# Performance work log

Measured on AMD Instinct MI355X. Metric: run time of the kernel, lower is better.

## Reference

```python
import jax, jax.numpy as jnp
import numpy as np

N = 100000
E = 1600000
D_IN = 128
D_H = 128


def setup_inputs() -> dict:
    key = jax.random.key(0)
    ks = jax.random.split(key, 8)
    x = jax.random.normal(ks[0], (N, D_IN), dtype=jnp.float32)
    edge_index = jax.random.randint(ks[1], (2, E), 0, N, dtype=jnp.int64)
    # Glorot-ish init for weights, zeros for biases (PyG GCNConv default: glorot W, zero bias)
    W1 = jax.random.normal(ks[2], (D_IN, D_H), dtype=jnp.float32) / np.sqrt(D_IN)
    b1 = jnp.zeros((D_H,), dtype=jnp.float32)
    W2 = jax.random.normal(ks[3], (D_H, D_H), dtype=jnp.float32) / np.sqrt(D_H)
    b2 = jnp.zeros((D_H,), dtype=jnp.float32)
    Wout = jax.random.normal(ks[4], (D_H, 1), dtype=jnp.float32) / np.sqrt(D_H)
    bout = jnp.zeros((1,), dtype=jnp.float32)
    return {"x": x, "edge_index": edge_index, "W1": W1, "b1": b1,
            "W2": W2, "b2": b2, "Wout": Wout, "bout": bout}


def _gcn_conv(x, W, b, src, dst, inv_sqrt_deg, inv_deg):
    # PyG GCNConv: h = x @ W; out = sum_{j in N(i)} norm_ij * h_j + (1/deg_i) * h_i + b
    # norm_ij = deg_i^-1/2 * deg_j^-1/2 with self-loops folded into deg.
    h = x @ W                                   # [N, D]
    norm = inv_sqrt_deg[src] * inv_sqrt_deg[dst]  # [E]
    msgs = h[src] * norm[:, None]               # [E, D] gather
    agg = jax.ops.segment_sum(msgs, dst, num_segments=x.shape[0])  # [N, D] scatter
    agg = agg + h * inv_deg[:, None]            # self-loop term (norm = 1/deg)
    return agg + b


def reference(x, edge_index, W1, b1, W2, b2, Wout, bout):
    src = edge_index[0]
    dst = edge_index[1]
    n = x.shape[0]
    # degree with self-loops: deg_i = 1 + #incoming edges to i
    deg = 1.0 + jax.ops.segment_sum(jnp.ones((src.shape[0],), dtype=x.dtype), dst, num_segments=n)
    inv_sqrt_deg = jax.lax.rsqrt(deg)
    inv_deg = 1.0 / deg
    h = jax.nn.relu(_gcn_conv(x, W1, b1, src, dst, inv_sqrt_deg, inv_deg))
    h = jax.nn.relu(_gcn_conv(h, W2, b2, src, dst, inv_sqrt_deg, inv_deg))
    logits = h @ Wout + bout                    # [N, 1]
    return jax.nn.sigmoid(logits).squeeze(-1)   # [N]
```

## Files before the change

kernel.cpp:

```cpp
#include <hip/hip_runtime.h>
#include <cstddef>

#define CAPD 64
#define BSZ 512
#define BSH 9
#define CHUNK 8192
#define BCAP 12288

typedef unsigned int uint;
typedef unsigned short ushort;
typedef unsigned char uchar;
typedef float f32x4 __attribute__((ext_vector_type(4)));
typedef _Float16 f16x8 __attribute__((ext_vector_type(8)));

__device__ inline float h_lo(uint v) {
    union { ushort u; _Float16 h; } c; c.u = (ushort)(v & 0xFFFFu); return (float)c.h;
}
__device__ inline float h_hi(uint v) {
    union { ushort u; _Float16 h; } c; c.u = (ushort)(v >> 16); return (float)c.h;
}
__device__ inline ushort h_bits(float x) {
    union { _Float16 h; ushort u; } c; c.h = (_Float16)x; return c.u;
}
__device__ inline uint h_pack(float a, float b) {
    return (uint)h_bits(a) | ((uint)h_bits(b) << 16);
}
__device__ inline float ub0(uint v) { return (float)(v & 0xFFu); }
__device__ inline float ub1(uint v) { return (float)((v >> 8) & 0xFFu); }
__device__ inline float ub2(uint v) { return (float)((v >> 16) & 0xFFu); }
__device__ inline float ub3(uint v) { return (float)(v >> 24); }

__global__ __launch_bounds__(256) void p3_scatter(const int* __restrict__ esrc,
                                                  const int* __restrict__ edst, int E,
                                                  int nb, int NB2,
                                                  int* __restrict__ bucketCursor,
                                                  unsigned* __restrict__ gSorted,
                                                  const float* __restrict__ W1,
                                                  const float* __restrict__ W2,
                                                  uint* __restrict__ Wt1,
                                                  uint* __restrict__ Wt2) {
    __shared__ __align__(16) char SHB[78848];
    int bid = blockIdx.x, tid = threadIdx.x;
    if (bid >= NB2) {
        const float* W = (bid - NB2) ? W2 : W1;
        uint* O = (bid - NB2) ? Wt2 : Wt1;
        float (*ws)[129] = (float(*)[129])SHB;
#pragma unroll
        for (int j = 0; j < 16; ++j) {
            int q = tid + 256 * j;
            int k = q >> 5, c = (q & 31) * 4;
            float4 v = *reinterpret_cast<const float4*>(W + k * 128 + c);
            ws[k][c] = v.x; ws[k][c + 1] = v.y; ws[k][c + 2] = v.z; ws[k][c + 3] = v.w;
        }
        __syncthreads();
#pragma unroll
        for (int j = 0; j < 32; ++j) {
            int q = tid + 256 * j;
            int ncol = q >> 6, kw = q & 63;
            O[q] = h_pack(ws[2 * kw][ncol], ws[2 * kw + 1][ncol]);
        }
        return;
    }
    uint*  payL = (uint*)SHB;
    uint*  outL = (uint*)(SHB + 32768);
    uchar* bktL = (uchar*)(SHB + 65536);
    int*   hist   = (int*)(SHB + 73728);
    int*   segoff = hist + 256;
    int*   cursor = segoff + 256;
    int*   gbase  = cursor + 256;
    int*   sc     = gbase + 256;
    int e0 = bid * CHUNK;
    int m = min(E - e0, CHUNK);
    for (int i = tid; i < m; i += 256) {
        unsigned d = (unsigned)edst[e0 + i];
        unsigned s = (unsigned)esrc[e0 + i];
        payL[i] = s | ((d & (BSZ - 1)) << 23);
        bktL[i] = (uchar)(d >> BSH);
    }
    hist[tid] = 0;
    __syncthreads();
    for (int i = tid; i < m; i += 256)
        atomicAdd(&hist[bktL[i]], 1);
    __syncthreads();
    sc[tid] = hist[tid];
    __syncthreads();
    for (int off = 1; off < 256; off <<= 1) {
        int v = (tid >= off) ? sc[tid - off] : 0;
        __syncthreads();
        sc[tid] += v;
        __syncthreads();
    }
    segoff[tid] = sc[tid] - hist[tid];
    cursor[tid] = segoff[tid];
    if (tid < nb && hist[tid] > 0) gbase[tid] = atomicAdd(&bucketCursor[tid], hist[tid]);
    __syncthreads();
    for (int i = tid; i < m; i += 256) {
        int b = (int)bktL[i];
        int p = atomicAdd(&cursor[b], 1);
        outL[p] = payL[i];
    }
    __syncthreads();
    int wave = tid >> 6, lane = tid & 63;
    for (int b = wave; b < nb; b += 4) {
        int off = segoff[b], len = hist[b];
        if (len == 0) continue;
        int gb = gbase[b];
        unsigned* dst = gSorted + (size_t)b * BCAP;
        for (int i = lane; i < len; i += 64)
            if (gb + i < BCAP) dst[gb + i] = outL[off + i];
    }
}

__device__ __forceinline__ void gemm_core(const void* __restrict__ A, int aF16,
                                          const uint* __restrict__ Wt,
                                          const float* __restrict__ scale,
                                          uint* __restrict__ Tq,
                                          float* __restrict__ Ts,
                                          int n, int m0, int tid, uint* SH) {
    char* shb = (char*)SH;
    if (aF16) {
        const uint* Af = (const uint*)A;
#pragma unroll
        for (int j = 0; j < 8; ++j) {
            int q = tid + 256 * j;
            int row = q >> 4, c16 = q & 15;
            int grow = m0 + row;
            uint4 v = make_uint4(0u, 0u, 0u, 0u);
            if (grow < n) v = *reinterpret_cast<const uint4*>(Af + (size_t)grow * 64 + c16 * 4);
            *reinterpret_cast<uint4*>(shb + row * 256 + ((c16 * 16) ^ ((row & 7) << 4))) = v;
        }
    } else {
        const float* Af = (const float*)A;
#pragma unroll
        for (int j = 0; j < 8; ++j) {
            int q = tid + 256 * j;
            int row = q >> 4, c16 = q & 15;
            int grow = m0 + row;
            uint4 o = make_uint4(0u, 0u, 0u, 0u);
            if (grow < n) {
                float4 v0 = *reinterpret_cast<const float4*>(Af + (size_t)grow * 128 + c16 * 8);
                float4 v1 = *reinterpret_cast<const float4*>(Af + (size_t)grow * 128 + c16 * 8 + 4);
                o.x = h_pack(v0.x, v0.y); o.y = h_pack(v0.z, v0.w);
                o.z = h_pack(v1.x, v1.y); o.w = h_pack(v1.z, v1.w);
            }
            *reinterpret_cast<uint4*>(shb + row * 256 + ((c16 * 16) ^ ((row & 7) << 4))) = o;
        }
    }
#pragma unroll
    for (int j = 0; j < 8; ++j) {
        int q = tid + 256 * j;
        int col = q >> 4, c16 = q & 15;
        uint4 v = *reinterpret_cast<const uint4*>(Wt + col * 64 + c16 * 4);
        *reinterpret_cast<uint4*>(shb + 32768 + col * 256 + ((c16 * 16) ^ ((col & 7) << 4))) = v;
    }
    __syncthreads();

    const int w = tid >> 6, l = tid & 63;
    const int lrow = l & 15, kg = l >> 4;
    const int swz = (lrow & 7) << 4;

    f32x4 acc[2][8] = {};
#pragma unroll
    for (int kk = 0; kk < 4; ++kk) {
        const int koff = (kk * 64 + kg * 16) ^ swz;
        f16x8 a[2], b[8];
#pragma unroll
        for (int mr = 0; mr < 2; ++mr) {
            int r = w * 32 + mr * 16 + lrow;
            a[mr] = *reinterpret_cast<const f16x8*>(shb + r * 256 + koff);
        }
#pragma unroll
        for (int nc = 0; nc < 8; ++nc) {
            int c = nc * 16 + lrow;
            b[nc] = *reinterpret_cast<const f16x8*>(shb + 32768 + c * 256 + koff);
        }
#pragma unroll
        for (int mr = 0; mr < 2; ++mr)
#pragma unroll
            for (int nc = 0; nc < 8; ++nc)
                acc[mr][nc] = __builtin_amdgcn_mfma_f32_16x16x32_f16(a[mr], b[nc], acc[mr][nc], 0, 0, 0);
    }
    __syncthreads();

    ushort* Cs = (ushort*)SH;
#pragma unroll
    for (int mr = 0; mr < 2; ++mr) {
        int rb = w * 32 + mr * 16 + kg * 4;
#pragma unroll
        for (int i = 0; i < 4; ++i) {
            int grow = m0 + rb + i;
            float s = scale ? ((grow < n) ? scale[grow] : 0.f) : 1.f;
#pragma unroll
            for (int nc = 0; nc < 8; ++nc)
                Cs[(rb + i) * 136 + nc * 16 + lrow] = h_bits(s * acc[mr][nc][i]);
        }
    }
    __syncthreads();
    const uint* Cw = (const uint*)SH;
#pragma unroll
    for (int j = 0; j < 8; ++j) {
        int q = tid + 256 * j;
        int row = q >> 4, c8 = q & 15;
        int grow = m0 + row;
        uint4 v = *reinterpret_cast<const uint4*>(Cw + row * 68 + c8 * 4);
        float f0 = h_lo(v.x), f1 = h_hi(v.x), f2 = h_lo(v.y), f3 = h_hi(v.y);
        float f4 = h_lo(v.z), f5 = h_hi(v.z), f6 = h_lo(v.w), f7 = h_hi(v.w);
        float mx = fmaxf(fmaxf(fmaxf(fabsf(f0), fabsf(f1)), fmaxf(fabsf(f2), fabsf(f3))),
                         fmaxf(fmaxf(fabsf(f4), fabsf(f5)), fmaxf(fabsf(f6), fabsf(f7))));
#pragma unroll
        for (int off = 8; off > 0; off >>= 1) mx = fmaxf(mx, __shfl_xor(mx, off, 16));
        mx = fmaxf(mx, 1e-20f);
        float inv = 127.f / mx;
        int q0 = (int)rintf(f0 * inv) + 128, q1 = (int)rintf(f1 * inv) + 128;
        int q2 = (int)rintf(f2 * inv) + 128, q3 = (int)rintf(f3 * inv) + 128;
        int q4 = (int)rintf(f4 * inv) + 128, q5 = (int)rintf(f5 * inv) + 128;
        int q6 = (int)rintf(f6 * inv) + 128, q7 = (int)rintf(f7 * inv) + 128;
        uint w0 = (uint)q0 | ((uint)q1 << 8) | ((uint)q2 << 16) | ((uint)q3 << 24);
        uint w1 = (uint)q4 | ((uint)q5 << 8) | ((uint)q6 << 16) | ((uint)q7 << 24);
        if (grow < n) {
            *reinterpret_cast<uint2*>(Tq + (size_t)grow * 32 + c8 * 2) = make_uint2(w0, w1);
            if (c8 == 0) Ts[grow] = mx * (1.f / 127.f);
        }
    }
}

__global__ __launch_bounds__(256) void p4_mega(const unsigned* __restrict__ gSorted,
                                               const int* __restrict__ bucketCursor,
                                               int nb, int N,
                                               int* __restrict__ cnt,
                                               float* __restrict__ isd,
                                               int* __restrict__ ell,
                                               const float* __restrict__ x,
                                               const uint* __restrict__ Wt1,
                                               uint* __restrict__ Tq,
                                               float* __restrict__ Ts) {
    __shared__ __align__(16) uint SH[16384];
    __shared__ int cntL[256];
    int bid = blockIdx.x, tid = threadIdx.x;
    if (bid < 2 * nb) {
        int bucket = bid >> 1;
        unsigned half = (unsigned)(bid & 1);
        int n0 = bid * 256;
        uint* ellL = SH;
        cntL[tid] = 0;
        __syncthreads();
        int len = bucketCursor[bucket];
        if (len > BCAP) len = BCAP;
        const unsigned* seg = gSorted + (size_t)bucket * BCAP;
        for (int i = tid; i < len; i += 256) {
            unsigned e = seg[i];
            unsigned dl = e >> 23;
            if ((dl >> 8) == half) {
                int r = (int)(dl & 255u);
                int p = atomicAdd(&cntL[r], 1);
                if (p < CAPD) ellL[r * CAPD + p] = e & 0x7FFFFFu;
            }
        }
        __syncthreads();
        int nValid = min(256, N - n0);
        if (nValid > 0) {
            int total = nValid * CAPD;
            const int* ellLi = (const int*)ellL;
            for (int i = tid; i < total; i += 256) {
                int row = i >> 6, pos = i & 63;
                int c = cntL[row];
                if (pos < min(c, CAPD))
                    ell[(size_t)n0 * CAPD + i] = ellLi[i];
            }
            for (int i = tid; i < nValid; i += 256) {
                int c = cntL[i];
                cnt[n0 + i] = c;
                isd[n0 + i] = rsqrtf(1.0f + (float)c);
            }
        }
    } else {
        gemm_core(x, 0, Wt1, nullptr, Tq, Ts, N, (bid - 2 * nb) * 128, tid, SH);
    }
}

__global__ __launch_bounds__(256) void tsc_kernel(const float* __restrict__ Ts,
                                                  const float* __restrict__ isd,
                                                  float* __restrict__ Tsc, int n4) {
    int i = (blockIdx.x * 256 + threadIdx.x) * 4;
    if (i >= n4 * 4) return;
    float4 a = *reinterpret_cast<const float4*>(Ts + i);
    float4 b = *reinterpret_cast<const float4*>(isd + i);
    float4 o = make_float4(a.x * b.x, a.y * b.y, a.z * b.z, a.w * b.w);
    *reinterpret_cast<float4*>(Tsc + i) = o;
}

__global__ __launch_bounds__(256) void gemm2_kernel(const uint* __restrict__ Hb,
                                                    const uint* __restrict__ Wt,
                                                    const float* __restrict__ isd,
                                                    uint* __restrict__ Tq,
                                                    float* __restrict__ Ts, int n) {
    __shared__ __align__(16) uint SH[16384];
    gemm_core(Hb, 1, Wt, isd, Tq, Ts, n, blockIdx.x * 128, threadIdx.x, SH);
}

__global__ __launch_bounds__(256) void agg_kernel(const uint* __restrict__ Tq,
                                                  const float* __restrict__ Tsc,
                                                  const int* __restrict__ ell,
                                                  const int* __restrict__ cnt,
                                                  const float* __restrict__ isd,
                                                  const float* __restrict__ bias,
                                                  uint* __restrict__ Hb, int n) {
    int node = (int)((blockIdx.x * 256 + threadIdx.x) >> 5);
    int ln = threadIdx.x & 31;
    if (node >= n) return;
    float di = isd[node];
    int c = cnt[node];
    if (c > CAPD) c = CAPD;
    const int* row = ell + (size_t)node * CAPD;
    float a0, a1, a2, a3, ssum;
    {
        uint v = Tq[(size_t)node * 32 + ln];
        float sc = Tsc[node];
        ssum = sc;
        a0 = sc * ub0(v); a1 = sc * ub1(v); a2 = sc * ub2(v); a3 = sc * ub3(v);
    }
    int j = 0;
    for (; j + 8 <= c; j += 8) {
        int4 sa = *reinterpret_cast<const int4*>(row + j);
        int4 sb = *reinterpret_cast<const int4*>(row + j + 4);
        uint v0 = Tq[(size_t)sa.x * 32 + ln]; float c0 = Tsc[sa.x];
        uint v1 = Tq[(size_t)sa.y * 32 + ln]; float c1 = Tsc[sa.y];
        uint v2 = Tq[(size_t)sa.z * 32 + ln]; float c2 = Tsc[sa.z];
        uint v3 = Tq[(size_t)sa.w * 32 + ln]; float c3 = Tsc[sa.w];
        uint v4 = Tq[(size_t)sb.x * 32 + ln]; float c4 = Tsc[sb.x];
        uint v5 = Tq[(size_t)sb.y * 32 + ln]; float c5 = Tsc[sb.y];
        uint v6 = Tq[(size_t)sb.z * 32 + ln]; float c6 = Tsc[sb.z];
        uint v7 = Tq[(size_t)sb.w * 32 + ln]; float c7 = Tsc[sb.w];
        ssum += ((c0 + c1) + (c2 + c3)) + ((c4 + c5) + (c6 + c7));
        a0 = fmaf(c0, ub0(v0), fmaf(c1, ub0(v1), fmaf(c2, ub0(v2), fmaf(c3, ub0(v3),
             fmaf(c4, ub0(v4), fmaf(c5, ub0(v5), fmaf(c6, ub0(v6), fmaf(c7, ub0(v7), a0))))))));
        a1 = fmaf(c0, ub1(v0), fmaf(c1, ub1(v1), fmaf(c2, ub1(v2), fmaf(c3, ub1(v3),
             fmaf(c4, ub1(v4), fmaf(c5, ub1(v5), fmaf(c6, ub1(v6), fmaf(c7, ub1(v7), a1))))))));
        a2 = fmaf(c0, ub2(v0), fmaf(c1, ub2(v1), fmaf(c2, ub2(v2), fmaf(c3, ub2(v3),
             fmaf(c4, ub2(v4), fmaf(c5, ub2(v5), fmaf(c6, ub2(v6), fmaf(c7, ub2(v7), a2))))))));
        a3 = fmaf(c0, ub3(v0), fmaf(c1, ub3(v1), fmaf(c2, ub3(v2), fmaf(c3, ub3(v3),
             fmaf(c4, ub3(v4), fmaf(c5, ub3(v5), fmaf(c6, ub3(v6), fmaf(c7, ub3(v7), a3))))))));
    }
    for (; j + 4 <= c; j += 4) {
        int4 s4 = *reinterpret_cast<const int4*>(row + j);
        uint v0 = Tq[(size_t)s4.x * 32 + ln]; float c0 = Tsc[s4.x];
        uint v1 = Tq[(size_t)s4.y * 32 + ln]; float c1 = Tsc[s4.y];
        uint v2 = Tq[(size_t)s4.z * 32 + ln]; float c2 = Tsc[s4.z];
        uint v3 = Tq[(size_t)s4.w * 32 + ln]; float c3 = Tsc[s4.w];
        ssum += (c0 + c1) + (c2 + c3);
        a0 = fmaf(c0, ub0(v0), fmaf(c1, ub0(v1), fmaf(c2, ub0(v2), fmaf(c3, ub0(v3), a0))));
        a1 = fmaf(c0, ub1(v0), fmaf(c1, ub1(v1), fmaf(c2, ub1(v2), fmaf(c3, ub1(v3), a1))));
        a2 = fmaf(c0, ub2(v0), fmaf(c1, ub2(v1), fmaf(c2, ub2(v2), fmaf(c3, ub2(v3), a2))));
        a3 = fmaf(c0, ub3(v0), fmaf(c1, ub3(v1), fmaf(c2, ub3(v2), fmaf(c3, ub3(v3), a3))));
    }
    for (; j < c; ++j) {
        int s = row[j];
        uint v = Tq[(size_t)s * 32 + ln];
        float sc = Tsc[s];
        ssum += sc;
        a0 = fmaf(sc, ub0(v), a0); a1 = fmaf(sc, ub1(v), a1);
        a2 = fmaf(sc, ub2(v), a2); a3 = fmaf(sc, ub3(v), a3);
    }
    float off = 128.f * ssum;
    float4 bv = *reinterpret_cast<const float4*>(bias + ln * 4);
    float h0 = fmaxf(fmaf(di, a0 - off, bv.x), 0.f);
    float h1 = fmaxf(fmaf(di, a1 - off, bv.y), 0.f);
    float h2 = fmaxf(fmaf(di, a2 - off, bv.z), 0.f);
    float h3 = fmaxf(fmaf(di, a3 - off, bv.w), 0.f);
    *reinterpret_cast<uint2*>(Hb + (size_t)node * 64 + ln * 2) =
        make_uint2(h_pack(h0, h1), h_pack(h2, h3));
}

__global__ __launch_bounds__(256) void agg_out_kernel(const uint* __restrict__ Tq,
                                                      const float* __restrict__ Ts,
                                                      const int* __restrict__ ell,
                                                      const int* __restrict__ cnt,
                                                      const float* __restrict__ isd,
                                                      const float* __restrict__ bias,
                                                      const float* __restrict__ Wout,
                                                      const float* __restrict__ bout,
                                                      float* __restrict__ out, int n) {
    int node = (int)((blockIdx.x * 256 + threadIdx.x) >> 5);
    int ln = threadIdx.x & 31;
    if (node >= n) return;
    float di = isd[node];
    int c = cnt[node];
    if (c > CAPD) c = CAPD;
    const int* row = ell + (size_t)node * CAPD;
    float a0, a1, a2, a3, ssum;
    {
        uint v = Tq[(size_t)node * 32 + ln];
        float sc = Ts[node];
        ssum = sc;
        a0 = sc * ub0(v); a1 = sc * ub1(v); a2 = sc * ub2(v); a3 = sc * ub3(v);
    }
    int j = 0;
    for (; j + 8 <= c; j += 8) {
        int4 sa = *reinterpret_cast<const int4*>(row + j);
        int4 sb = *reinterpret_cast<const int4*>(row + j + 4);
        uint v0 = Tq[(size_t)sa.x * 32 + ln]; float c0 = Ts[sa.x];
        uint v1 = Tq[(size_t)sa.y * 32 + ln]; float c1 = Ts[sa.y];
        uint v2 = Tq[(size_t)sa.z * 32 + ln]; float c2 = Ts[sa.z];
        uint v3 = Tq[(size_t)sa.w * 32 + ln]; float c3 = Ts[sa.w];
        uint v4 = Tq[(size_t)sb.x * 32 + ln]; float c4 = Ts[sb.x];
        uint v5 = Tq[(size_t)sb.y * 32 + ln]; float c5 = Ts[sb.y];
        uint v6 = Tq[(size_t)sb.z * 32 + ln]; float c6 = Ts[sb.z];
        uint v7 = Tq[(size_t)sb.w * 32 + ln]; float c7 = Ts[sb.w];
        ssum += ((c0 + c1) + (c2 + c3)) + ((c4 + c5) + (c6 + c7));
        a0 = fmaf(c0, ub0(v0), fmaf(c1, ub0(v1), fmaf(c2, ub0(v2), fmaf(c3, ub0(v3),
             fmaf(c4, ub0(v4), fmaf(c5, ub0(v5), fmaf(c6, ub0(v6), fmaf(c7, ub0(v7), a0))))))));
        a1 = fmaf(c0, ub1(v0), fmaf(c1, ub1(v1), fmaf(c2, ub1(v2), fmaf(c3, ub1(v3),
             fmaf(c4, ub1(v4), fmaf(c5, ub1(v5), fmaf(c6, ub1(v6), fmaf(c7, ub1(v7), a1))))))));
        a2 = fmaf(c0, ub2(v0), fmaf(c1, ub2(v1), fmaf(c2, ub2(v2), fmaf(c3, ub2(v3),
             fmaf(c4, ub2(v4), fmaf(c5, ub2(v5), fmaf(c6, ub2(v6), fmaf(c7, ub2(v7), a2))))))));
        a3 = fmaf(c0, ub3(v0), fmaf(c1, ub3(v1), fmaf(c2, ub3(v2), fmaf(c3, ub3(v3),
             fmaf(c4, ub3(v4), fmaf(c5, ub3(v5), fmaf(c6, ub3(v6), fmaf(c7, ub3(v7), a3))))))));
    }
    for (; j + 4 <= c; j += 4) {
        int4 s4 = *reinterpret_cast<const int4*>(row + j);
        uint v0 = Tq[(size_t)s4.x * 32 + ln]; float c0 = Ts[s4.x];
        uint v1 = Tq[(size_t)s4.y * 32 + ln]; float c1 = Ts[s4.y];
        uint v2 = Tq[(size_t)s4.z * 32 + ln]; float c2 = Ts[s4.z];
        uint v3 = Tq[(size_t)s4.w * 32 + ln]; float c3 = Ts[s4.w];
        ssum += (c0 + c1) + (c2 + c3);
        a0 = fmaf(c0, ub0(v0), fmaf(c1, ub0(v1), fmaf(c2, ub0(v2), fmaf(c3, ub0(v3), a0))));
        a1 = fmaf(c0, ub1(v0), fmaf(c1, ub1(v1), fmaf(c2, ub1(v2), fmaf(c3, ub1(v3), a1))));
        a2 = fmaf(c0, ub2(v0), fmaf(c1, ub2(v1), fmaf(c2, ub2(v2), fmaf(c3, ub2(v3), a2))));
        a3 = fmaf(c0, ub3(v0), fmaf(c1, ub3(v1), fmaf(c2, ub3(v2), fmaf(c3, ub3(v3), a3))));
    }
    for (; j < c; ++j) {
        int s = row[j];
        uint v = Tq[(size_t)s * 32 + ln];
        float sc = Ts[s];
        ssum += sc;
        a0 = fmaf(sc, ub0(v), a0); a1 = fmaf(sc, ub1(v), a1);
        a2 = fmaf(sc, ub2(v), a2); a3 = fmaf(sc, ub3(v), a3);
    }
    float off = 128.f * ssum;
    float4 bv = *reinterpret_cast<const float4*>(bias + ln * 4);
    float4 wv = *reinterpret_cast<const float4*>(Wout + ln * 4);
    float h0 = fmaxf(fmaf(di, a0 - off, bv.x), 0.f);
    float h1 = fmaxf(fmaf(di, a1 - off, bv.y), 0.f);
    float h2 = fmaxf(fmaf(di, a2 - off, bv.z), 0.f);
    float h3 = fmaxf(fmaf(di, a3 - off, bv.w), 0.f);
    float v = fmaf(h0, wv.x, fmaf(h1, wv.y, fmaf(h2, wv.z, h3 * wv.w)));
#pragma unroll
    for (int off2 = 16; off2 > 0; off2 >>= 1) v += __shfl_xor(v, off2, 32);
    if (ln == 0) out[node] = 1.f / (1.f + expf(-(v + bout[0])));
}

extern "C" void kernel_launch(void* const* d_in, const int* in_sizes, int n_in,
                              void* d_out, int out_size, void* d_ws, size_t ws_size,
                              hipStream_t stream) {
    const float* x    = (const float*)d_in[0];
    const int*   ei   = (const int*)d_in[1];
    const float* W1   = (const float*)d_in[2];
    const float* b1   = (const float*)d_in[3];
    const float* W2   = (const float*)d_in[4];
    const float* b2   = (const float*)d_in[5];
    const float* Wout = (const float*)d_in[6];
    const float* bout = (const float*)d_in[7];
    float* out = (float*)d_out;

    const int N = in_sizes[0] / 128;
    const int E = in_sizes[1] / 2;
    const int* esrc = ei;
    const int* edst = ei + E;

    char* p = (char*)d_ws;
    auto alloc = [&](size_t bytes) {
        char* r = p;
        p += (bytes + 255) & ~(size_t)255;
        return (void*)r;
    };
    const int nb  = (N + BSZ - 1) / BSZ;
    const int NB2 = (E + CHUNK - 1) / CHUNK;

    int*   cnt = (int*)  alloc((size_t)N * 4);
    float* isd = (float*)alloc((size_t)N * 4);
    int*   ell = (int*)  alloc((size_t)N * CAPD * 4);
    uint*  Tq  = (uint*) alloc((size_t)N * 32 * 4);
    float* Ts  = (float*)alloc((size_t)(N + 4) * 4);
    float* Tsc = (float*)alloc((size_t)(N + 4) * 4);
    uint*  Hb  = (uint*) alloc((size_t)N * 64 * 4);
    uint*  Wt1 = (uint*) alloc(8192 * 4);
    uint*  Wt2 = (uint*) alloc(8192 * 4);
    unsigned* gSorted      = (unsigned*)alloc((size_t)nb * BCAP * 4);
    int*      bucketCursor = (int*)     alloc((size_t)nb * 4);

    hipMemsetAsync(bucketCursor, 0, (size_t)nb * 4, stream);
    p3_scatter<<<NB2 + 2, 256, 0, stream>>>(esrc, edst, E, nb, NB2, bucketCursor, gSorted,
                                            W1, W2, Wt1, Wt2);

    const int gblocks = (N + 127) / 128;
    const int ablocks = (N + 7) / 8;
    p4_mega<<<2 * nb + gblocks, 256, 0, stream>>>(gSorted, bucketCursor, nb, N,
                                                  cnt, isd, ell, x, Wt1, Tq, Ts);
    const int n4 = (N + 3) / 4;
    tsc_kernel<<<(n4 + 255) / 256, 256, 0, stream>>>(Ts, isd, Tsc, n4);
    agg_kernel<<<ablocks, 256, 0, stream>>>(Tq, Tsc, ell, cnt, isd, b1, Hb, N);
    gemm2_kernel<<<gblocks, 256, 0, stream>>>(Hb, Wt2, isd, Tq, Ts, N);
    agg_out_kernel<<<ablocks, 256, 0, stream>>>(Tq, Ts, ell, cnt, isd, b2, Wout, bout, out, N);
}
```

Before: 178.2 us.

## Split ELL build from GEMM1, fuse Tsc scaling into GEMM1 epilogue

The combined ELL-build plus GEMM1 kernel is split in two. A separate ELL build kernel now uses 128-node sub-buckets, four per bucket, so it needs less shared memory and launches more blocks. GEMM1 then runs after it and computes Tsc = Ts*isd directly in its epilogue, which removes the separate tsc kernel launch and its pass over memory. The cost is that the two phases no longer overlap within a single launch, and each bucket segment is now scanned four times instead of twice.

Measured after the change: 188.5 us. +5.7%, slower.

```diff
diff --git a/kernel.cpp b/kernel.cpp
--- a/kernel.cpp
+++ b/kernel.cpp
@@ -111,11 +111,56 @@
     }
 }
 
+__global__ __launch_bounds__(256) void p4_build(const unsigned* __restrict__ gSorted,
+                                                const int* __restrict__ bucketCursor,
+                                                int nb, int N, int* __restrict__ cnt,
+                                                float* __restrict__ isd,
+                                                int* __restrict__ ell) {
+    __shared__ unsigned ellL[128 * CAPD];
+    __shared__ int cntL[128];
+    int bid = blockIdx.x, tid = threadIdx.x;
+    int bucket = bid >> 2;
+    unsigned sub = (unsigned)(bid & 3);
+    int n0 = bid * 128;
+    int nValid = min(128, N - n0);
+    if (nValid <= 0) return;
+    for (int i = tid; i < 128; i += 256) cntL[i] = 0;
+    __syncthreads();
+    int len = bucketCursor[bucket];
+    if (len > BCAP) len = BCAP;
+    const unsigned* seg = gSorted + (size_t)bucket * BCAP;
+    for (int i = tid; i < len; i += 256) {
+        unsigned e = seg[i];
+        unsigned dl = e >> 23;
+        if ((dl >> 7) == sub) {
+            int r = (int)(dl & 127u);
+            int p = atomicAdd(&cntL[r], 1);
+            if (p < CAPD) ellL[r * CAPD + p] = e & 0x7FFFFFu;
+        }
+    }
+    __syncthreads();
+    int total = nValid * CAPD;
+    const int* ellLi = (const int*)ellL;
+    for (int i = tid; i < total; i += 256) {
+        int row = i >> 6, pos = i & 63;
+        int c = cntL[row];
+        if (pos < min(c, CAPD))
+            ell[(size_t)n0 * CAPD + i] = ellLi[i];
+    }
+    for (int i = tid; i < nValid; i += 256) {
+        int c = cntL[i];
+        cnt[n0 + i] = c;
+        isd[n0 + i] = rsqrtf(1.0f + (float)c);
+    }
+}
+
 __device__ __forceinline__ void gemm_core(const void* __restrict__ A, int aF16,
                                           const uint* __restrict__ Wt,
                                           const float* __restrict__ scale,
+                                          const float* __restrict__ isdT,
                                           uint* __restrict__ Tq,
                                           float* __restrict__ Ts,
+                                          float* __restrict__ TscOut,
                                           int n, int m0, int tid, uint* SH) {
     char* shb = (char*)SH;
     if (aF16) {
@@ -219,74 +264,23 @@
         uint w1 = (uint)q4 | ((uint)q5 << 8) | ((uint)q6 << 16) | ((uint)q7 << 24);
         if (grow < n) {
             *reinterpret_cast<uint2*>(Tq + (size_t)grow * 32 + c8 * 2) = make_uint2(w0, w1);
-            if (c8 == 0) Ts[grow] = mx * (1.f / 127.f);
-        }
-    }
-}
-
-__global__ __launch_bounds__(256) void p4_mega(const unsigned* __restrict__ gSorted,
-                                               const int* __restrict__ bucketCursor,
-                                               int nb, int N,
-                                               int* __restrict__ cnt,
-                                               float* __restrict__ isd,
-                                               int* __restrict__ ell,
-                                               const float* __restrict__ x,
-                                               const uint* __restrict__ Wt1,
-                                               uint* __restrict__ Tq,
-                                               float* __restrict__ Ts) {
+            if (c8 == 0) {
+                float ts = mx * (1.f / 127.f);
+                Ts[grow] = ts;
+                if (TscOut) TscOut[grow] = ts * isdT[grow];
+            }
+        }
+    }
+}
+
+__global__ __launch_bounds__(256) void gemm1_kernel(const float* __restrict__ x,
+                                                    const uint* __restrict__ Wt,
+                                                    const float* __restrict__ isd,
+                                                    uint* __restrict__ Tq,
+                                                    float* __restrict__ Ts,
+                                                    float* __restrict__ Tsc, int n) {
     __shared__ __align__(16) uint SH[16384];
-    __shared__ int cntL[256];
-    int bid = blockIdx.x, tid = threadIdx.x;
-    if (bid < 2 * nb) {
-        int bucket = bid >> 1;
-        unsigned half = (unsigned)(bid & 1);
-        int n0 = bid * 256;
-        uint* ellL = SH;
-        cntL[tid] = 0;
-        __syncthreads();
-        int len = bucketCursor[bucket];
-        if (len > BCAP) len = BCAP;
-        const unsigned* seg = gSorted + (size_t)bucket * BCAP;
-        for (int i = tid; i < len; i += 256) {
-            unsigned e = seg[i];
-            unsigned dl = e >> 23;
-            if ((dl >> 8) == half) {
-                int r = (int)(dl & 255u);
-                int p = atomicAdd(&cntL[r], 1);
-                if (p < CAPD) ellL[r * CAPD + p] = e & 0x7FFFFFu;
-            }
-        }
-        __syncthreads();
-        int nValid = min(256, N - n0);
-        if (nValid > 0) {
-            int total = nValid * CAPD;
-            const int* ellLi = (const int*)ellL;
-            for (int i = tid; i < total; i += 256) {
-                int row = i >> 6, pos = i & 63;
-                int c = cntL[row];
-                if (pos < min(c, CAPD))
-                    ell[(size_t)n0 * CAPD + i] = ellLi[i];
-            }
-            for (int i = tid; i < nValid; i += 256) {
-                int c = cntL[i];
-                cnt[n0 + i] = c;
-                isd[n0 + i] = rsqrtf(1.0f + (float)c);
-            }
-        }
-    } else {
-        gemm_core(x, 0, Wt1, nullptr, Tq, Ts, N, (bid - 2 * nb) * 128, tid, SH);
-    }
-}
-
-__global__ __launch_bounds__(256) void tsc_kernel(const float* __restrict__ Ts,
-                                                  const float* __restrict__ isd,
-                                                  float* __restrict__ Tsc, int n4) {
-    int i = (blockIdx.x * 256 + threadIdx.x) * 4;
-    if (i >= n4 * 4) return;
-    float4 a = *reinterpret_cast<const float4*>(Ts + i);
-    float4 b = *reinterpret_cast<const float4*>(isd + i);
-    float4 o = make_float4(a.x * b.x, a.y * b.y, a.z * b.z, a.w * b.w);
-    *reinterpret_cast<float4*>(Tsc + i) = o;
+    gemm_core(x, 0, Wt, nullptr, isd, Tq, Ts, Tsc, n, blockIdx.x * 128, threadIdx.x, SH);
 }
 
 __global__ __launch_bounds__(256) void gemm2_kernel(const uint* __restrict__ Hb,
@@ -295,7 +289,7 @@
                                                     uint* __restrict__ Tq,
                                                     float* __restrict__ Ts, int n) {
     __shared__ __align__(16) uint SH[16384];
-    gemm_core(Hb, 1, Wt, isd, Tq, Ts, n, blockIdx.x * 128, threadIdx.x, SH);
+    gemm_core(Hb, 1, Wt, isd, nullptr, Tq, Ts, nullptr, n, blockIdx.x * 128, threadIdx.x, SH);
 }
 
 __global__ __launch_bounds__(256) void agg_kernel(const uint* __restrict__ Tq,
@@ -491,13 +485,11 @@
     hipMemsetAsync(bucketCursor, 0, (size_t)nb * 4, stream);
     p3_scatter<<<NB2 + 2, 256, 0, stream>>>(esrc, edst, E, nb, NB2, bucketCursor, gSorted,
                                             W1, W2, Wt1, Wt2);
+    p4_build<<<4 * nb, 256, 0, stream>>>(gSorted, bucketCursor, nb, N, cnt, isd, ell);
 
     const int gblocks = (N + 127) / 128;
     const int ablocks = (N + 7) / 8;
-    p4_mega<<<2 * nb + gblocks, 256, 0, stream>>>(gSorted, bucketCursor, nb, N,
-                                                  cnt, isd, ell, x, Wt1, Tq, Ts);
-    const int n4 = (N + 3) / 4;
-    tsc_kernel<<<(n4 + 255) / 256, 256, 0, stream>>>(Ts, isd, Tsc, n4);
+    gemm1_kernel<<<gblocks, 256, 0, stream>>>(x, Wt1, isd, Tq, Ts, Tsc, N);
     agg_kernel<<<ablocks, 256, 0, stream>>>(Tq, Tsc, ell, cnt, isd, b1, Hb, N);
     gemm2_kernel<<<gblocks, 256, 0, stream>>>(Hb, Wt2, isd, Tq, Ts, N);
     agg_out_kernel<<<ablocks, 256, 0, stream>>>(Tq, Ts, ell, cnt, isd, b2, Wout, bout, out, N);
```
